# Kernel optimization log

Measured on AMD Instinct MI355X. Metric: run time of the kernel, lower is better.

## Reference

```python
import jax, jax.numpy as jnp
import numpy as np

B, CIN, HIN, WIN = 1, 26, 721, 1440
K, HOUT, KH, KW = 9, 360, 9, 9
COUT = 256
PSCALE = WIN // (WIN // 2)  # lon downsample stride = 2
WOUT = WIN // 2


def setup_inputs() -> dict:
    key = jax.random.key(0)
    k1, k2, k3 = jax.random.split(key, 3)
    x = jax.random.normal(k1, (B, CIN, HIN, WIN), dtype=jnp.float32)
    # precomputed basis*quadrature stencil psi[k, ho, dh, dw] (shift-invariant in lon,
    # stored only for wo=0, exactly as DISCO does). Normalized per (k, ho) ('mean' mode).
    psi = jax.random.normal(k2, (K, HOUT, KH, KW), dtype=jnp.float32)
    psi = psi / (jnp.mean(jnp.abs(psi), axis=(2, 3), keepdims=True) * (KH * KW) + 1e-6)
    weight = jax.random.normal(k3, (COUT, CIN, K), dtype=jnp.float32) * (1.0 / np.sqrt(CIN * K))
    # base input-lat row for each output lat (stencil top row), clipped to valid range
    hi_base = np.clip(np.round(np.arange(HOUT) * (HIN - 1) / HOUT).astype(np.int32) - KH // 2, 0, HIN - 1)
    return {"x": x, "psi": psi, "weight": weight, "hi_base": jnp.asarray(hi_base, dtype=jnp.int32)}


def _disco_conv(x, psi, weight, hi_base):
    x = x.astype(jnp.float32)  # fp32 autocast-off region, matches torch module
    acc = jnp.zeros((B, CIN, K, HOUT, WOUT), dtype=jnp.float32)
    for dh in range(KH):  # small structural loop over stencil rows
        rows = jnp.clip(hi_base + dh, 0, HIN - 1)  # [Hout]
        xr = x[:, :, rows, :]
        for dw in range(KW):  # small structural loop over stencil lon offsets
            shift = dw - KW // 2
            xs = jnp.roll(xr, -shift, axis=-1)[..., ::PSCALE]  # [B,C,Hout,Wout]
            acc = acc + psi[:, :, dh, dw][None, None, :, :, None] * xs[:, :, None, :, :]
    # contract learned weights over kernel basis and input channels
    out = jnp.einsum('bckhw,ock->bohw', acc, weight)  # [B,Cout,Hout,Wout]
    return out


def reference(x, psi, weight, hi_base):
    return _disco_conv(x, psi, weight, hi_base)
```

## Files before the change

kernel.cpp:

```cpp
#include <hip/hip_runtime.h>
#include <hip/hip_bf16.h>

#define CIN_   26
#define HIN_   721
#define WIN_   1440
#define K_     9
#define HOUT_  360
#define KH_    9
#define KW_    9
#define COUT_  256
#define WOUT_  720

#define WT     16
#define XSP    42
#define CK     (CIN_ * K_)
#define KPAD2  288
#define NKS2   9
#define ACCP2  296
#define NMT    (COUT_ / 16)
#define NXCD   8
#define HBAND  (HOUT_ / NXCD)
#define NSTG   19

typedef short bf16x8 __attribute__((ext_vector_type(8)));
typedef float f32x4  __attribute__((ext_vector_type(4)));

__device__ unsigned short g_whi[NMT * NKS2 * 64 * 8];
__device__ unsigned short g_pfrag[HOUT_ * 3 * 64 * 8];

__device__ __forceinline__ unsigned short f2bf_rne(float f) {
    union { float f; unsigned u; } v; v.f = f;
    unsigned u = v.u;
    unsigned r = (u + 0x7FFFu + ((u >> 16) & 1u)) >> 16;
    return (unsigned short)r;
}
__device__ __forceinline__ unsigned pack_bf2(float a, float b) {
    const __hip_bfloat162 bv = __float22bfloat162_rn(make_float2(a, b));
    return *reinterpret_cast<const unsigned*>(&bv);
}

__global__ void prep_weight_kernel(const float* __restrict__ weight) {
    const int bid  = blockIdx.x;
    const int mt   = bid / NKS2;
    const int ks   = bid % NKS2;
    const int lane = threadIdx.x;
    const int row  = mt * 16 + (lane & 15);
    const int k0   = ks * 32 + (lane >> 4) * 8;
    const int base = ((mt * NKS2 + ks) * 64 + lane) * 8;
    #pragma unroll
    for (int j = 0; j < 8; ++j) {
        const int kp = k0 + j;
        float w = 0.f;
        if (kp < 260) {
            const int c = kp / 10, m = kp % 10;
            if (m < 9) w = weight[row * CK + c * 9 + m];
        }
        g_whi[base + j] = f2bf_rne(w);
    }
}

__global__ void prep_psi_kernel(const float* __restrict__ psi) {
    const int h    = blockIdx.x;
    const int lane = threadIdx.x;
    const int m    = lane & 15;
    const int kg   = lane >> 4;
    #pragma unroll
    for (int ks = 0; ks < 3; ++ks) {
        const int base = ((h * 3 + ks) * 64 + lane) * 8;
        #pragma unroll
        for (int e = 0; e < 8; ++e) {
            const int s = ks * 32 + kg * 8 + e;
            float v = 0.f;
            if (m < 9) {
                if (s < 72)      v = psi[(m * HOUT_ + h) * 81 + (s >> 3) * 9 + (s & 7)];
                else if (s < 81) v = psi[(m * HOUT_ + h) * 81 + (s - 72) * 9 + 8];
            }
            g_pfrag[base + e] = f2bf_rne(v);
        }
    }
}

__global__ __launch_bounds__(256, 4)
void disco_fused_kernel(const float* __restrict__ x,
                        const int*   __restrict__ hi_base,
                        float* __restrict__ out)
{
    __shared__ unsigned short xs_bf[CK][XSP];
    __shared__ __align__(16) unsigned short acc_s[WT][ACCP2];

    const int b    = blockIdx.x;
    const int xcd  = b & (NXCD - 1);
    const int jb   = b >> 3;
    const int h    = xcd * HBAND + jb / 45;
    const int tile = jb % 45;
    const int w0   = tile * WT;
    const int tid  = threadIdx.x;

    const int hib = hi_base[h];

    #pragma unroll
    for (int t = 0; t < 2; ++t) {
        const int e = tid + t * 256;
        if (e < 16 * 28) acc_s[e / 28][260 + e % 28] = 0;
    }

    const int c0 = 2 * w0 - 4;
    float2 sv[NSTG];
    int    soff[NSTG];
    #pragma unroll
    for (int t = 0; t < NSTG; ++t) {
        const int i = tid + t * 256;
        const bool valid = (i < CK * 20);
        const int ii  = valid ? i : 0;
        const int p   = ii % 20;
        const int row = ii / 20;
        const int dh  = row % KH_;
        const int c   = row / KH_;
        int r = hib + dh;
        if (r > HIN_ - 1) r = HIN_ - 1;
        int g = c0 + 2 * p;
        if (g < 0)          g += WIN_;
        else if (g >= WIN_) g -= WIN_;
        sv[t]   = *reinterpret_cast<const float2*>(x + ((size_t)c * HIN_ + r) * WIN_ + g);
        soff[t] = valid ? (row * XSP + 2 * p) : -1;
    }
    #pragma unroll
    for (int t = 0; t < NSTG; ++t) {
        if (soff[t] >= 0)
            *reinterpret_cast<unsigned*>(&xs_bf[0][0] + soff[t]) = pack_bf2(sv[t].x, sv[t].y);
    }

    const int lane = tid & 63;
    const int wid  = tid >> 6;
    const int n    = lane & 15;
    const int kg   = lane >> 4;

    bf16x8 afrag[3];
    #pragma unroll
    for (int ks = 0; ks < 3; ++ks)
        afrag[ks] = *(const bf16x8*)&g_pfrag[((h * 3 + ks) * 64 + lane) * 8];

    __syncthreads();

    const char* xsb = (const char*)&xs_bf[0][0];
    for (int c = wid; c < CIN_; c += 4) {
        const int base = c * (KH_ * XSP * 2) + 4 * n;
        f32x4 C = {0.f, 0.f, 0.f, 0.f};
        #pragma unroll
        for (int ks = 0; ks < 3; ++ks) {
            union { bf16x8 v; unsigned d[4]; unsigned short u[8]; } bf;
            if (ks < 2 || kg == 0) {
                const char* p = xsb + base + (ks * 4 + kg) * (XSP * 2);
                #pragma unroll
                for (int t = 0; t < 4; ++t)
                    bf.d[t] = *(const unsigned*)(p + 4 * t);
            } else if (kg == 1) {
                #pragma unroll
                for (int e = 0; e < 8; ++e)
                    bf.u[e] = *(const unsigned short*)(xsb + base + e * (XSP * 2) + 16);
            } else if (kg == 2) {
                bf.d[0] = bf.d[1] = bf.d[2] = bf.d[3] = 0;
                bf.u[0] = *(const unsigned short*)(xsb + base + 8 * (XSP * 2) + 16);
            } else {
                bf.d[0] = bf.d[1] = bf.d[2] = bf.d[3] = 0;
            }
            C = __builtin_amdgcn_mfma_f32_16x16x32_bf16(afrag[ks], bf.v, C, 0, 0, 0);
        }
        if (kg < 2) {
            unsigned* ap = reinterpret_cast<unsigned*>(&acc_s[n][c * 10 + kg * 4]);
            ap[0] = pack_bf2(C[0], C[1]);
            ap[1] = pack_bf2(C[2], C[3]);
        } else if (kg == 2) {
            *reinterpret_cast<unsigned*>(&acc_s[n][c * 10 + 8]) = pack_bf2(C[0], 0.f);
        }
    }
    __syncthreads();

    f32x4 C0 = {0.f, 0.f, 0.f, 0.f};
    f32x4 C1 = C0, C2 = C0, C3 = C0;

    const unsigned short* wp = g_whi + ((size_t)(wid * 4) * NKS2 * 64 + lane) * 8;

    bf16x8 wc[4];
    #pragma unroll
    for (int i = 0; i < 4; ++i)
        wc[i] = *(const bf16x8*)(wp + (size_t)i * NKS2 * 512);

    #pragma unroll
    for (int ks = 0; ks < NKS2; ++ks) {
        bf16x8 wn[4];
        if (ks + 1 < NKS2) {
            #pragma unroll
            for (int i = 0; i < 4; ++i)
                wn[i] = *(const bf16x8*)(wp + ((size_t)i * NKS2 + (ks + 1)) * 512);
        }
        const bf16x8 bhi = *(const bf16x8*)&acc_s[n][ks * 32 + kg * 8];
        C0 = __builtin_amdgcn_mfma_f32_16x16x32_bf16(wc[0], bhi, C0, 0, 0, 0);
        C1 = __builtin_amdgcn_mfma_f32_16x16x32_bf16(wc[1], bhi, C1, 0, 0, 0);
        C2 = __builtin_amdgcn_mfma_f32_16x16x32_bf16(wc[2], bhi, C2, 0, 0, 0);
        C3 = __builtin_amdgcn_mfma_f32_16x16x32_bf16(wc[3], bhi, C3, 0, 0, 0);
        if (ks + 1 < NKS2) {
            #pragma unroll
            for (int i = 0; i < 4; ++i) wc[i] = wn[i];
        }
    }

    #pragma unroll
    for (int i = 0; i < 4; ++i) {
        const f32x4 acc = (i == 0) ? C0 : (i == 1) ? C1 : (i == 2) ? C2 : C3;
        const int m0 = (wid * 4 + i) * 16 + kg * 4;
        #pragma unroll
        for (int r = 0; r < 4; ++r) {
            out[(size_t)(m0 + r) * (HOUT_ * WOUT_) + h * WOUT_ + w0 + n] = acc[r];
        }
    }
}

extern "C" void kernel_launch(void* const* d_in, const int* in_sizes, int n_in,
                              void* d_out, int out_size, void* d_ws, size_t ws_size,
                              hipStream_t stream)
{
    const float* x       = (const float*)d_in[0];
    const float* psi     = (const float*)d_in[1];
    const float* weight  = (const float*)d_in[2];
    const int*   hi_base = (const int*)d_in[3];
    float* out = (float*)d_out;

    hipLaunchKernelGGL(prep_weight_kernel, dim3(NMT * NKS2), dim3(64), 0, stream, weight);
    hipLaunchKernelGGL(prep_psi_kernel,    dim3(HOUT_),      dim3(64), 0, stream, psi);

    dim3 grid(45 * HOUT_, 1, 1);
    dim3 block(256, 1, 1);
    hipLaunchKernelGGL(disco_fused_kernel, grid, block, 0, stream,
                       x, hi_base, out);
}
```

Baseline: 265.8 us.

## Split fused DISCO kernel into stencil phase and batched channel-mixing GEMM

The single fused kernel becomes two. The first computes the psi-stencil contraction per tile and writes the bf16 intermediate to a global buffer already laid out as MFMA fragments. The second kernel processes four tiles per block, so each weight fragment loaded from global memory is reused across more output columns. This cuts repeated weight loads and lets the stencil phase run at higher occupancy, at the cost of a roughly 150 MB global round trip for the intermediate and an extra kernel launch.

```diff
diff --git a/kernel.cpp b/kernel.cpp
--- a/kernel.cpp
+++ b/kernel.cpp
@@ -14,19 +14,20 @@
 #define WT     16
 #define XSP    42
 #define CK     (CIN_ * K_)
-#define KPAD2  288
 #define NKS2   9
-#define ACCP2  296
 #define NMT    (COUT_ / 16)
 #define NXCD   8
 #define HBAND  (HOUT_ / NXCD)
 #define NSTG   19
+#define NTILE  16200
+#define NT4    4
 
 typedef short bf16x8 __attribute__((ext_vector_type(8)));
 typedef float f32x4  __attribute__((ext_vector_type(4)));
 
 __device__ unsigned short g_whi[NMT * NKS2 * 64 * 8];
 __device__ unsigned short g_pfrag[HOUT_ * 3 * 64 * 8];
+__device__ unsigned short g_acc[(size_t)NTILE * 4608];
 
 __device__ __forceinline__ unsigned short f2bf_rne(float f) {
     union { float f; unsigned u; } v; v.f = f;
@@ -80,13 +81,11 @@
     }
 }
 
-__global__ __launch_bounds__(256, 4)
-void disco_fused_kernel(const float* __restrict__ x,
-                        const int*   __restrict__ hi_base,
-                        float* __restrict__ out)
+__global__ __launch_bounds__(256, 8)
+void disco_phase1_kernel(const float* __restrict__ x,
+                         const int*   __restrict__ hi_base)
 {
     __shared__ unsigned short xs_bf[CK][XSP];
-    __shared__ __align__(16) unsigned short acc_s[WT][ACCP2];
 
     const int b    = blockIdx.x;
     const int xcd  = b & (NXCD - 1);
@@ -94,22 +93,17 @@
     const int h    = xcd * HBAND + jb / 45;
     const int tile = jb % 45;
     const int w0   = tile * WT;
+    const int t    = h * 45 + tile;
     const int tid  = threadIdx.x;
 
     const int hib = hi_base[h];
-
-    #pragma unroll
-    for (int t = 0; t < 2; ++t) {
-        const int e = tid + t * 256;
-        if (e < 16 * 28) acc_s[e / 28][260 + e % 28] = 0;
-    }
 
     const int c0 = 2 * w0 - 4;
     float2 sv[NSTG];
     int    soff[NSTG];
     #pragma unroll
-    for (int t = 0; t < NSTG; ++t) {
-        const int i = tid + t * 256;
+    for (int tt = 0; tt < NSTG; ++tt) {
+        const int i = tid + tt * 256;
         const bool valid = (i < CK * 20);
         const int ii  = valid ? i : 0;
         const int p   = ii % 20;
@@ -121,13 +115,13 @@
         int g = c0 + 2 * p;
         if (g < 0)          g += WIN_;
         else if (g >= WIN_) g -= WIN_;
-        sv[t]   = *reinterpret_cast<const float2*>(x + ((size_t)c * HIN_ + r) * WIN_ + g);
-        soff[t] = valid ? (row * XSP + 2 * p) : -1;
-    }
-    #pragma unroll
-    for (int t = 0; t < NSTG; ++t) {
-        if (soff[t] >= 0)
-            *reinterpret_cast<unsigned*>(&xs_bf[0][0] + soff[t]) = pack_bf2(sv[t].x, sv[t].y);
+        sv[tt]   = *reinterpret_cast<const float2*>(x + ((size_t)c * HIN_ + r) * WIN_ + g);
+        soff[tt] = valid ? (row * XSP + 2 * p) : -1;
+    }
+    #pragma unroll
+    for (int tt = 0; tt < NSTG; ++tt) {
+        if (soff[tt] >= 0)
+            *reinterpret_cast<unsigned*>(&xs_bf[0][0] + soff[tt]) = pack_bf2(sv[tt].x, sv[tt].y);
     }
 
     const int lane = tid & 63;
@@ -140,8 +134,17 @@
     for (int ks = 0; ks < 3; ++ks)
         afrag[ks] = *(const bf16x8*)&g_pfrag[((h * 3 + ks) * 64 + lane) * 8];
 
+    if (tid < 224) {
+        const int j  = tid >> 4, nn = tid & 15;
+        const int kp = 260 + 2 * j;
+        const int ks2 = kp >> 5, kg2 = (kp >> 3) & 3, e = kp & 7;
+        unsigned short* p = g_acc + ((size_t)(t * 9 + ks2) * 4 + kg2) * 128 + nn * 8 + e;
+        *reinterpret_cast<unsigned*>(p) = 0u;
+    }
+
     __syncthreads();
 
+    const size_t t9 = (size_t)t * 9;
     const char* xsb = (const char*)&xs_bf[0][0];
     for (int c = wid; c < CIN_; c += 4) {
         const int base = c * (KH_ * XSP * 2) + 4 * n;
@@ -152,8 +155,8 @@
             if (ks < 2 || kg == 0) {
                 const char* p = xsb + base + (ks * 4 + kg) * (XSP * 2);
                 #pragma unroll
-                for (int t = 0; t < 4; ++t)
-                    bf.d[t] = *(const unsigned*)(p + 4 * t);
+                for (int tt = 0; tt < 4; ++tt)
+                    bf.d[tt] = *(const unsigned*)(p + 4 * tt);
             } else if (kg == 1) {
                 #pragma unroll
                 for (int e = 0; e < 8; ++e)
@@ -167,17 +170,43 @@
             C = __builtin_amdgcn_mfma_f32_16x16x32_bf16(afrag[ks], bf.v, C, 0, 0, 0);
         }
         if (kg < 2) {
-            unsigned* ap = reinterpret_cast<unsigned*>(&acc_s[n][c * 10 + kg * 4]);
-            ap[0] = pack_bf2(C[0], C[1]);
-            ap[1] = pack_bf2(C[2], C[3]);
+            const int kp0 = c * 10 + kg * 4;
+            {
+                const int ks2 = kp0 >> 5, kg2 = (kp0 >> 3) & 3, e = kp0 & 7;
+                unsigned short* p = g_acc + ((t9 + ks2) * 4 + kg2) * 128 + n * 8 + e;
+                *reinterpret_cast<unsigned*>(p) = pack_bf2(C[0], C[1]);
+            }
+            {
+                const int kp2 = kp0 + 2;
+                const int ks2 = kp2 >> 5, kg2 = (kp2 >> 3) & 3, e = kp2 & 7;
+                unsigned short* p = g_acc + ((t9 + ks2) * 4 + kg2) * 128 + n * 8 + e;
+                *reinterpret_cast<unsigned*>(p) = pack_bf2(C[2], C[3]);
+            }
         } else if (kg == 2) {
-            *reinterpret_cast<unsigned*>(&acc_s[n][c * 10 + 8]) = pack_bf2(C[0], 0.f);
-        }
-    }
-    __syncthreads();
-
-    f32x4 C0 = {0.f, 0.f, 0.f, 0.f};
-    f32x4 C1 = C0, C2 = C0, C3 = C0;
+            const int kp = c * 10 + 8;
+            const int ks2 = kp >> 5, kg2 = (kp >> 3) & 3, e = kp & 7;
+            unsigned short* p = g_acc + ((t9 + ks2) * 4 + kg2) * 128 + n * 8 + e;
+            *reinterpret_cast<unsigned*>(p) = pack_bf2(C[0], 0.f);
+        }
+    }
+}
+
+__global__ __launch_bounds__(256, 4)
+void disco_gemm_kernel(float* __restrict__ out)
+{
+    const int b4   = blockIdx.x;
+    const int tid  = threadIdx.x;
+    const int lane = tid & 63;
+    const int wid  = tid >> 6;
+    const int n    = lane & 15;
+    const int kg   = lane >> 4;
+
+    f32x4 C[NT4][4];
+    #pragma unroll
+    for (int q = 0; q < NT4; ++q)
+        #pragma unroll
+        for (int i = 0; i < 4; ++i)
+            C[q][i] = (f32x4){0.f, 0.f, 0.f, 0.f};
 
     const unsigned short* wp = g_whi + ((size_t)(wid * 4) * NKS2 * 64 + lane) * 8;
 
@@ -186,7 +215,6 @@
     for (int i = 0; i < 4; ++i)
         wc[i] = *(const bf16x8*)(wp + (size_t)i * NKS2 * 512);
 
-    #pragma unroll
     for (int ks = 0; ks < NKS2; ++ks) {
         bf16x8 wn[4];
         if (ks + 1 < NKS2) {
@@ -194,11 +222,15 @@
             for (int i = 0; i < 4; ++i)
                 wn[i] = *(const bf16x8*)(wp + ((size_t)i * NKS2 + (ks + 1)) * 512);
         }
-        const bf16x8 bhi = *(const bf16x8*)&acc_s[n][ks * 32 + kg * 8];
-        C0 = __builtin_amdgcn_mfma_f32_16x16x32_bf16(wc[0], bhi, C0, 0, 0, 0);
-        C1 = __builtin_amdgcn_mfma_f32_16x16x32_bf16(wc[1], bhi, C1, 0, 0, 0);
-        C2 = __builtin_amdgcn_mfma_f32_16x16x32_bf16(wc[2], bhi, C2, 0, 0, 0);
-        C3 = __builtin_amdgcn_mfma_f32_16x16x32_bf16(wc[3], bhi, C3, 0, 0, 0);
+        #pragma unroll
+        for (int q = 0; q < NT4; ++q) {
+            const int t = b4 * NT4 + q;
+            const bf16x8 bq = *(const bf16x8*)(g_acc + ((size_t)(t * 9 + ks) * 4 + kg) * 128 + n * 8);
+            C[q][0] = __builtin_amdgcn_mfma_f32_16x16x32_bf16(wc[0], bq, C[q][0], 0, 0, 0);
+            C[q][1] = __builtin_amdgcn_mfma_f32_16x16x32_bf16(wc[1], bq, C[q][1], 0, 0, 0);
+            C[q][2] = __builtin_amdgcn_mfma_f32_16x16x32_bf16(wc[2], bq, C[q][2], 0, 0, 0);
+            C[q][3] = __builtin_amdgcn_mfma_f32_16x16x32_bf16(wc[3], bq, C[q][3], 0, 0, 0);
+        }
         if (ks + 1 < NKS2) {
             #pragma unroll
             for (int i = 0; i < 4; ++i) wc[i] = wn[i];
@@ -206,12 +238,17 @@
     }
 
     #pragma unroll
-    for (int i = 0; i < 4; ++i) {
-        const f32x4 acc = (i == 0) ? C0 : (i == 1) ? C1 : (i == 2) ? C2 : C3;
-        const int m0 = (wid * 4 + i) * 16 + kg * 4;
-        #pragma unroll
-        for (int r = 0; r < 4; ++r) {
-            out[(size_t)(m0 + r) * (HOUT_ * WOUT_) + h * WOUT_ + w0 + n] = acc[r];
+    for (int q = 0; q < NT4; ++q) {
+        const int t  = b4 * NT4 + q;
+        const int h  = t / 45;
+        const int w0 = (t % 45) * WT;
+        #pragma unroll
+        for (int i = 0; i < 4; ++i) {
+            const int m0 = (wid * 4 + i) * 16 + kg * 4;
+            #pragma unroll
+            for (int r = 0; r < 4; ++r) {
+                out[(size_t)(m0 + r) * (HOUT_ * WOUT_) + h * WOUT_ + w0 + n] = C[q][i][r];
+            }
         }
     }
 }
@@ -229,8 +266,6 @@
     hipLaunchKernelGGL(prep_weight_kernel, dim3(NMT * NKS2), dim3(64), 0, stream, weight);
     hipLaunchKernelGGL(prep_psi_kernel,    dim3(HOUT_),      dim3(64), 0, stream, psi);
 
-    dim3 grid(45 * HOUT_, 1, 1);
-    dim3 block(256, 1, 1);
-    hipLaunchKernelGGL(disco_fused_kernel, grid, block, 0, stream,
-                       x, hi_base, out);
-}
+    hipLaunchKernelGGL(disco_phase1_kernel, dim3(NTILE), dim3(256), 0, stream, x, hi_base);
+    hipLaunchKernelGGL(disco_gemm_kernel,   dim3(NTILE / NT4), dim3(256), 0, stream, out);
+}
```

Measured after the change: 408.2 us. +53.6%, slower.
